# Kernel optimization log

Measured on AMD Instinct MI355X. Metric: run time of the kernel, lower is better.

## Reference

```python
import jax, jax.numpy as jnp
import numpy as np

B, L, E, D, A = 32, 2048, 1024, 1024, 1024

def setup_inputs() -> dict:
    key = jax.random.key(0)
    k1, k2, k3, k4, k5 = jax.random.split(key, 5)
    s_e = 1.0 / np.sqrt(E)
    s_d = 1.0 / np.sqrt(D)
    s_a = 1.0 / np.sqrt(A)
    return {
        "encoder_outputs": jax.random.normal(k1, (B, L, E), dtype=jnp.float32),
        "decoder_hidden": jax.random.normal(k2, (B, D), dtype=jnp.float32),
        "mask": jnp.ones((B, L), dtype=jnp.int32),
        # nn.Linear weights are [out, in]; uniform(-1/sqrt(in), 1/sqrt(in))
        "W1": jax.random.uniform(k3, (A, E), jnp.float32, -s_e, s_e),
        "W2": jax.random.uniform(k4, (A, D), jnp.float32, -s_d, s_d),
        "v": jax.random.uniform(k5, (1, A), jnp.float32, -s_a, s_a),
    }

def reference(encoder_outputs, decoder_hidden, mask, W1, W2, v):
    # enc_t: [B,L,A], dec_t: [B,1,A]
    enc_t = jnp.einsum('ble,ae->bla', encoder_outputs, W1)
    dec_t = jnp.einsum('bd,ad->ba', decoder_hidden, W2)[:, None, :]
    combined = jnp.tanh(enc_t + dec_t)                       # [B,L,A]
    scores = jnp.einsum('bla,a->bl', combined, v[0])          # [B,L]
    scores = jnp.where(mask == 0, -jnp.inf, scores)
    attn = jax.nn.softmax(scores, axis=-1)                    # [B,L]
    context = jnp.einsum('bl,ble->be', attn, encoder_outputs) # [B,E]
    return (context, attn)
```

## Files before the change

kernel.cpp:

```cpp
#include <hip/hip_runtime.h>
#include <stdint.h>

typedef __bf16 bf16x8 __attribute__((ext_vector_type(8)));
typedef float f32x4 __attribute__((ext_vector_type(4)));
typedef unsigned short ushort8v __attribute__((ext_vector_type(8)));

__device__ __forceinline__ void gload_lds16(const void* g, void* l) {
  __builtin_amdgcn_global_load_lds(
      (const __attribute__((address_space(1))) void*)g,
      (__attribute__((address_space(3))) void*)l, 16, 0, 0);
}

__device__ __forceinline__ unsigned short f2bf(float f) {
  union { float f; unsigned int u; } x; x.f = f;
  unsigned int r = x.u + 0x7FFFu + ((x.u >> 16) & 1u);
  return (unsigned short)(r >> 16);
}

__device__ __forceinline__ float ftanh(float x) {
  float ax = fabsf(x);
  float e = __expf(-2.0f * ax);
  float r = (1.0f - e) / (1.0f + e);
  return copysignf(r, x);
}

__global__ __launch_bounds__(256) void w1cvt_kernel(
    const float* __restrict__ W1, unsigned short* __restrict__ w1b) {
  const int g = blockIdx.x * 256 + threadIdx.x;
  const int chunk = g >> 10;
  const int d16 = g & 1023;
  const int col = d16 >> 2, s = d16 & 3;
  const int np = chunk >> 5, ks = chunk & 31;
  const float* src = W1 + (size_t)(np * 256 + col) * 1024 + ks * 32 +
                     ((s ^ ((col >> 1) & 3)) * 8);
  const float4 v0 = *(const float4*)src;
  const float4 v1 = *(const float4*)(src + 4);
  ushort8v o;
  o[0] = f2bf(v0.x); o[1] = f2bf(v0.y); o[2] = f2bf(v0.z); o[3] = f2bf(v0.w);
  o[4] = f2bf(v1.x); o[5] = f2bf(v1.y); o[6] = f2bf(v1.z); o[7] = f2bf(v1.w);
  *((ushort8v*)w1b + g) = o;
}

__global__ __launch_bounds__(256) void dec_proj_kernel(
    const float* __restrict__ dec, const float* __restrict__ W2,
    float* __restrict__ u) {
  __shared__ __align__(16) float w2s[1024];
  const int a = blockIdx.x;
  const int t = threadIdx.x;
  *(float4*)(w2s + t * 4) = *(const float4*)(W2 + (size_t)a * 1024 + t * 4);
  __syncthreads();
  const int wid = t >> 6, l = t & 63;
  for (int bi = 0; bi < 8; ++bi) {
    const int b = wid * 8 + bi;
    const float* dp = dec + (size_t)b * 1024;
    float acc = 0.f;
#pragma unroll
    for (int i = 0; i < 4; ++i) {
      const int k = i * 256 + l * 4;
      const float4 dv = *(const float4*)(dp + k);
      const float4 wv = *(const float4*)(w2s + k);
      acc = fmaf(dv.x, wv.x, acc); acc = fmaf(dv.y, wv.y, acc);
      acc = fmaf(dv.z, wv.z, acc); acc = fmaf(dv.w, wv.w, acc);
    }
#pragma unroll
    for (int m = 1; m < 64; m <<= 1) acc += __shfl_xor(acc, m, 64);
    if (l == 0) u[(size_t)b * 1024 + a] = acc;
  }
}

__global__ __launch_bounds__(256, 2) void scores_kernel(
    const float* __restrict__ enc, const unsigned short* __restrict__ w1b,
    const float* __restrict__ u, const float* __restrict__ vvec,
    float* __restrict__ spart) {
  __shared__ __align__(16) char Al[16384];
  __shared__ __align__(16) char Bl[32768];
  __shared__ __align__(16) float sred[256];

  const int t = threadIdx.x;
  const int bid = blockIdx.x;
  const int np = (bid >> 3) & 3;
  const int panel = (bid & 7) + ((bid >> 5) << 3);
  const int m0 = panel * 128;
  const int n0 = np * 256;
  const int b = panel >> 4;
  const int l = t & 63, wid = t >> 6;
  const int wr = wid >> 1, wc = wid & 1;
  const int lm = l & 15, lg = l >> 4;

  const int soff = (lg ^ ((lm >> 1) & 3)) * 16;
  const int abase = (wr * 64 + lm) * 64 + soff;
  const int bbase = (wc * 128 + lm) * 64 + soff;
  const char* w1base = (const char*)w1b + (size_t)(np * 32) * 16384;
  const float* ub = u + (size_t)b * 1024;

  const int row0 = t >> 2;
  const int s0 = t & 3;
  const int xo = (s0 ^ ((row0 >> 1) & 3)) * 8;
  const float* srcA = enc + (size_t)(m0 + row0) * 1024 + xo;
  const int adst = t * 16;

  f32x4 acc[4][8];
#pragma unroll
  for (int mi = 0; mi < 4; ++mi)
#pragma unroll
    for (int ni = 0; ni < 8; ++ni) acc[mi][ni] = (f32x4){0.f, 0.f, 0.f, 0.f};

#pragma unroll
  for (int i = 0; i < 4; ++i)
    gload_lds16(w1base + i * 4096 + t * 16, Bl + i * 4096 + t * 16);
  {
    const float4 p0 = *(const float4*)srcA;
    const float4 p1 = *(const float4*)(srcA + 4);
    const float4 p2 = *(const float4*)(srcA + 65536);
    const float4 p3 = *(const float4*)(srcA + 65540);
    ushort8v o0, o1;
    o0[0] = f2bf(p0.x); o0[1] = f2bf(p0.y); o0[2] = f2bf(p0.z); o0[3] = f2bf(p0.w);
    o0[4] = f2bf(p1.x); o0[5] = f2bf(p1.y); o0[6] = f2bf(p1.z); o0[7] = f2bf(p1.w);
    o1[0] = f2bf(p2.x); o1[1] = f2bf(p2.y); o1[2] = f2bf(p2.z); o1[3] = f2bf(p2.w);
    o1[4] = f2bf(p3.x); o1[5] = f2bf(p3.y); o1[6] = f2bf(p3.z); o1[7] = f2bf(p3.w);
    *(ushort8v*)(Al + adst) = o0;
    *(ushort8v*)(Al + 4096 + adst) = o1;
  }
  __syncthreads();

#pragma unroll 2
  for (int ks = 0; ks < 32; ++ks) {
    const int abuf = (ks & 1) * 8192;
    const int bbuf = (ks & 1) * 16384;
    float4 p0, p1, p2, p3;
    if (ks < 31) {
      const char* wn = w1base + (size_t)(ks + 1) * 16384;
#pragma unroll
      for (int i = 0; i < 4; ++i)
        gload_lds16(wn + i * 4096 + t * 16,
                    Bl + (bbuf ^ 16384) + i * 4096 + t * 16);
      const float* sa = srcA + (ks + 1) * 32;
      p0 = *(const float4*)sa;
      p1 = *(const float4*)(sa + 4);
      p2 = *(const float4*)(sa + 65536);
      p3 = *(const float4*)(sa + 65540);
    }
    bf16x8 af[4], bf[8];
#pragma unroll
    for (int mi = 0; mi < 4; ++mi)
      af[mi] = *(const bf16x8*)(Al + abuf + abase + mi * 1024);
#pragma unroll
    for (int ni = 0; ni < 8; ++ni)
      bf[ni] = *(const bf16x8*)(Bl + bbuf + bbase + ni * 1024);
    __builtin_amdgcn_s_setprio(1);
#pragma unroll
    for (int mi = 0; mi < 4; ++mi)
#pragma unroll
      for (int ni = 0; ni < 8; ++ni)
        acc[mi][ni] = __builtin_amdgcn_mfma_f32_16x16x32_bf16(
            af[mi], bf[ni], acc[mi][ni], 0, 0, 0);
    __builtin_amdgcn_s_setprio(0);
    if (ks < 31) {
      ushort8v o0, o1;
      o0[0] = f2bf(p0.x); o0[1] = f2bf(p0.y); o0[2] = f2bf(p0.z); o0[3] = f2bf(p0.w);
      o0[4] = f2bf(p1.x); o0[5] = f2bf(p1.y); o0[6] = f2bf(p1.z); o0[7] = f2bf(p1.w);
      o1[0] = f2bf(p2.x); o1[1] = f2bf(p2.y); o1[2] = f2bf(p2.z); o1[3] = f2bf(p2.w);
      o1[4] = f2bf(p3.x); o1[5] = f2bf(p3.y); o1[6] = f2bf(p3.z); o1[7] = f2bf(p3.w);
      *(ushort8v*)(Al + (abuf ^ 8192) + adst) = o0;
      *(ushort8v*)(Al + (abuf ^ 8192) + 4096 + adst) = o1;
    }
    __syncthreads();
  }

  float rowp[4][4];
#pragma unroll
  for (int mi = 0; mi < 4; ++mi)
#pragma unroll
    for (int j = 0; j < 4; ++j) rowp[mi][j] = 0.f;
#pragma unroll
  for (int ni = 0; ni < 8; ++ni) {
    const int colA = n0 + wc * 128 + ni * 16 + lm;
    const float uu = ub[colA], vv = vvec[colA];
#pragma unroll
    for (int mi = 0; mi < 4; ++mi)
#pragma unroll
      for (int j = 0; j < 4; ++j)
        rowp[mi][j] += ftanh(acc[mi][ni][j] + uu) * vv;
  }
#pragma unroll
  for (int m = 1; m < 16; m <<= 1)
#pragma unroll
    for (int mi = 0; mi < 4; ++mi)
#pragma unroll
      for (int j = 0; j < 4; ++j) rowp[mi][j] += __shfl_xor(rowp[mi][j], m, 64);
  if (lm == 0) {
#pragma unroll
    for (int mi = 0; mi < 4; ++mi)
#pragma unroll
      for (int j = 0; j < 4; ++j)
        sred[wc * 128 + wr * 64 + mi * 16 + lg * 4 + j] = rowp[mi][j];
  }
  __syncthreads();
  if (t < 128) {
    spart[(size_t)np * 65536 + m0 + t] = sred[t] + sred[128 + t];
  }
}

__global__ __launch_bounds__(256) void softmax_kernel(
    const float* __restrict__ spart, float* __restrict__ out,
    const int* __restrict__ mask) {
  __shared__ float wred[4];
  const int bidx = blockIdx.x;
  const int t = threadIdx.x;
  const int r8 = bidx * 2048 + t * 8;
  float* at = out + 32768 + (size_t)bidx * 2048;
  const int* mk = mask + (size_t)bidx * 2048;
  float v[8] = {0.f, 0.f, 0.f, 0.f, 0.f, 0.f, 0.f, 0.f};
#pragma unroll
  for (int np = 0; np < 4; ++np) {
    const float4 s0 = *(const float4*)(spart + (size_t)np * 65536 + r8);
    const float4 s1 = *(const float4*)(spart + (size_t)np * 65536 + r8 + 4);
    v[0] += s0.x; v[1] += s0.y; v[2] += s0.z; v[3] += s0.w;
    v[4] += s1.x; v[5] += s1.y; v[6] += s1.z; v[7] += s1.w;
  }
  const int4 q0 = *(const int4*)(mk + t * 8);
  const int4 q1 = *(const int4*)(mk + t * 8 + 4);
  int q[8] = {q0.x, q0.y, q0.z, q0.w, q1.x, q1.y, q1.z, q1.w};
  float mx = -3.0e38f;
#pragma unroll
  for (int j = 0; j < 8; ++j) if (q[j] != 0) mx = fmaxf(mx, v[j]);
#pragma unroll
  for (int m = 1; m < 64; m <<= 1) mx = fmaxf(mx, __shfl_xor(mx, m, 64));
  if ((t & 63) == 0) wred[t >> 6] = mx;
  __syncthreads();
  mx = fmaxf(fmaxf(wred[0], wred[1]), fmaxf(wred[2], wred[3]));
  __syncthreads();
  float pp[8]; float sum = 0.f;
#pragma unroll
  for (int j = 0; j < 8; ++j) {
    pp[j] = (q[j] != 0) ? __expf(v[j] - mx) : 0.f;
    sum += pp[j];
  }
#pragma unroll
  for (int m = 1; m < 64; m <<= 1) sum += __shfl_xor(sum, m, 64);
  if ((t & 63) == 0) wred[t >> 6] = sum;
  __syncthreads();
  sum = (wred[0] + wred[1]) + (wred[2] + wred[3]);
  const float inv = 1.0f / sum;
  const float4 o0 = {pp[0] * inv, pp[1] * inv, pp[2] * inv, pp[3] * inv};
  const float4 o1 = {pp[4] * inv, pp[5] * inv, pp[6] * inv, pp[7] * inv};
  *(float4*)(at + t * 8) = o0;
  *(float4*)(at + t * 8 + 4) = o1;
}

__global__ __launch_bounds__(256) void context_kernel(
    const float* __restrict__ enc, float* __restrict__ out) {
  __shared__ __align__(16) float attnS[2048];
  __shared__ __align__(16) float red[8 * 128];
  const int bid = blockIdx.x;
  const int b = bid >> 3, ec = bid & 7;
  const int e0 = ec * 128;
  const int t = threadIdx.x;
  const float* attn = out + 32768 + (size_t)b * 2048;
#pragma unroll
  for (int i = 0; i < 8; ++i) attnS[i * 256 + t] = attn[i * 256 + t];
  __syncthreads();
  const int el = (t & 31) * 4;
  const int ls = t >> 5;
  f32x4 acc = {0.f, 0.f, 0.f, 0.f};
  const float* ebase = enc + (size_t)b * 2048 * 1024 + e0 + el;
  for (int l2 = ls; l2 < 2048; l2 += 8) {
    const float a = attnS[l2];
    const float4 ev = *(const float4*)(ebase + (size_t)l2 * 1024);
    acc[0] = fmaf(a, ev.x, acc[0]);
    acc[1] = fmaf(a, ev.y, acc[1]);
    acc[2] = fmaf(a, ev.z, acc[2]);
    acc[3] = fmaf(a, ev.w, acc[3]);
  }
  *(f32x4*)(red + ls * 128 + el) = acc;
  __syncthreads();
  if (t < 128) {
    float s = 0.f;
#pragma unroll
    for (int i = 0; i < 8; ++i) s += red[i * 128 + t];
    out[(size_t)b * 1024 + e0 + t] = s;
  }
}

extern "C" void kernel_launch(void* const* d_in, const int* in_sizes, int n_in,
                              void* d_out, int out_size, void* d_ws,
                              size_t ws_size, hipStream_t stream) {
  const float* enc = (const float*)d_in[0];
  const float* dec = (const float*)d_in[1];
  const int* mask = (const int*)d_in[2];
  const float* W1 = (const float*)d_in[3];
  const float* W2 = (const float*)d_in[4];
  const float* v = (const float*)d_in[5];
  float* out = (float*)d_out;
  char* ws = (char*)d_ws;
  unsigned short* w1b = (unsigned short*)ws;
  float* u = (float*)(ws + (2u << 20));
  float* spart = (float*)(ws + (2u << 20) + (128u << 10));

  w1cvt_kernel<<<512, 256, 0, stream>>>(W1, w1b);
  dec_proj_kernel<<<1024, 256, 0, stream>>>(dec, W2, u);
  scores_kernel<<<2048, 256, 0, stream>>>(enc, w1b, u, v, spart);
  softmax_kernel<<<32, 256, 0, stream>>>(spart, out, mask);
  context_kernel<<<256, 256, 0, stream>>>(enc, out);
}
```

Measured before the change: 275.0 us.

## Pre-convert encoder outputs to bf16 and stream them via direct-to-LDS loads

Adds a pass that converts the full fp32 encoder tensor to bf16 in workspace. The scores GEMM then loads A tiles with global_load_lds instead of register loads plus in-loop conversion, and the context reduction reads the bf16 copy. This costs an extra full read of enc (256MB) and a 128MB write, and the context sum now uses bf16-rounded inputs. The new path only runs when the workspace is large enough, otherwise the old kernels run.

```diff
diff --git a/kernel.cpp b/kernel.cpp
--- a/kernel.cpp
+++ b/kernel.cpp
@@ -15,6 +15,11 @@
   union { float f; unsigned int u; } x; x.f = f;
   unsigned int r = x.u + 0x7FFFu + ((x.u >> 16) & 1u);
   return (unsigned short)(r >> 16);
+}
+
+__device__ __forceinline__ float bf2f(unsigned short h) {
+  union { unsigned int u; float f; } x; x.u = ((unsigned int)h) << 16;
+  return x.f;
 }
 
 __device__ __forceinline__ float ftanh(float x) {
@@ -22,6 +27,17 @@
   float e = __expf(-2.0f * ax);
   float r = (1.0f - e) / (1.0f + e);
   return copysignf(r, x);
+}
+
+__global__ __launch_bounds__(256) void enc_cvt_kernel(
+    const float* __restrict__ enc, unsigned short* __restrict__ enc16) {
+  const size_t g = ((size_t)blockIdx.x * 256 + threadIdx.x) * 8;
+  const float4 v0 = *(const float4*)(enc + g);
+  const float4 v1 = *(const float4*)(enc + g + 4);
+  ushort8v o;
+  o[0] = f2bf(v0.x); o[1] = f2bf(v0.y); o[2] = f2bf(v0.z); o[3] = f2bf(v0.w);
+  o[4] = f2bf(v1.x); o[5] = f2bf(v1.y); o[6] = f2bf(v1.z); o[7] = f2bf(v1.w);
+  *(ushort8v*)(enc16 + g) = o;
 }
 
 __global__ __launch_bounds__(256) void w1cvt_kernel(
@@ -68,10 +84,10 @@
   }
 }
 
-__global__ __launch_bounds__(256, 2) void scores_kernel(
-    const float* __restrict__ enc, const unsigned short* __restrict__ w1b,
-    const float* __restrict__ u, const float* __restrict__ vvec,
-    float* __restrict__ spart) {
+__global__ __launch_bounds__(256, 2) void scores_kernel_g(
+    const unsigned short* __restrict__ enc16,
+    const unsigned short* __restrict__ w1b, const float* __restrict__ u,
+    const float* __restrict__ vvec, float* __restrict__ spart) {
   __shared__ __align__(16) char Al[16384];
   __shared__ __align__(16) char Bl[32768];
   __shared__ __align__(16) float sred[256];
@@ -93,18 +109,122 @@
   const char* w1base = (const char*)w1b + (size_t)(np * 32) * 16384;
   const float* ub = u + (size_t)b * 1024;
 
+  const int row1 = t >> 2, slot1 = t & 3;
+  const char* asrc1 = (const char*)enc16 + (size_t)(m0 + row1) * 2048 +
+                      ((slot1 ^ ((row1 >> 1) & 3)) * 16);
+  const char* asrc2 = asrc1 + 64 * 2048;
+
+  f32x4 acc[4][8];
+#pragma unroll
+  for (int mi = 0; mi < 4; ++mi)
+#pragma unroll
+    for (int ni = 0; ni < 8; ++ni) acc[mi][ni] = (f32x4){0.f, 0.f, 0.f, 0.f};
+
+#pragma unroll
+  for (int i = 0; i < 4; ++i)
+    gload_lds16(w1base + i * 4096 + t * 16, Bl + i * 4096 + t * 16);
+  gload_lds16(asrc1, Al + t * 16);
+  gload_lds16(asrc2, Al + 4096 + t * 16);
+  __syncthreads();
+
+#pragma unroll 2
+  for (int ks = 0; ks < 32; ++ks) {
+    const int abuf = (ks & 1) * 8192;
+    const int bbuf = (ks & 1) * 16384;
+    if (ks < 31) {
+      const char* wn = w1base + (size_t)(ks + 1) * 16384;
+#pragma unroll
+      for (int i = 0; i < 4; ++i)
+        gload_lds16(wn + i * 4096 + t * 16,
+                    Bl + (bbuf ^ 16384) + i * 4096 + t * 16);
+      const int aoff = (ks + 1) * 64;
+      gload_lds16(asrc1 + aoff, Al + (abuf ^ 8192) + t * 16);
+      gload_lds16(asrc2 + aoff, Al + (abuf ^ 8192) + 4096 + t * 16);
+    }
+    bf16x8 af[4], bf[8];
+#pragma unroll
+    for (int mi = 0; mi < 4; ++mi)
+      af[mi] = *(const bf16x8*)(Al + abuf + abase + mi * 1024);
+#pragma unroll
+    for (int ni = 0; ni < 8; ++ni)
+      bf[ni] = *(const bf16x8*)(Bl + bbuf + bbase + ni * 1024);
+    __builtin_amdgcn_s_setprio(1);
+#pragma unroll
+    for (int mi = 0; mi < 4; ++mi)
+#pragma unroll
+      for (int ni = 0; ni < 8; ++ni)
+        acc[mi][ni] = __builtin_amdgcn_mfma_f32_16x16x32_bf16(
+            af[mi], bf[ni], acc[mi][ni], 0, 0, 0);
+    __builtin_amdgcn_s_setprio(0);
+    __syncthreads();
+  }
+
+  float rowp[4][4];
+#pragma unroll
+  for (int mi = 0; mi < 4; ++mi)
+#pragma unroll
+    for (int j = 0; j < 4; ++j) rowp[mi][j] = 0.f;
+#pragma unroll
+  for (int ni = 0; ni < 8; ++ni) {
+    const int colA = n0 + wc * 128 + ni * 16 + lm;
+    const float uu = ub[colA], vv = vvec[colA];
+#pragma unroll
+    for (int mi = 0; mi < 4; ++mi)
+#pragma unroll
+      for (int j = 0; j < 4; ++j)
+        rowp[mi][j] += ftanh(acc[mi][ni][j] + uu) * vv;
+  }
+#pragma unroll
+  for (int m = 1; m < 16; m <<= 1)
+#pragma unroll
+    for (int mi = 0; mi < 4; ++mi)
+#pragma unroll
+      for (int j = 0; j < 4; ++j) rowp[mi][j] += __shfl_xor(rowp[mi][j], m, 64);
+  if (lm == 0) {
+#pragma unroll
+    for (int mi = 0; mi < 4; ++mi)
+#pragma unroll
+      for (int j = 0; j < 4; ++j)
+        sred[wc * 128 + wr * 64 + mi * 16 + lg * 4 + j] = rowp[mi][j];
+  }
+  __syncthreads();
+  if (t < 128) {
+    spart[(size_t)np * 65536 + m0 + t] = sred[t] + sred[128 + t];
+  }
+}
+
+__global__ __launch_bounds__(256, 2) void scores_kernel(
+    const float* __restrict__ enc, const unsigned short* __restrict__ w1b,
+    const float* __restrict__ u, const float* __restrict__ vvec,
+    float* __restrict__ spart) {
+  __shared__ __align__(16) char Al[16384];
+  __shared__ __align__(16) char Bl[32768];
+  __shared__ __align__(16) float sred[256];
+  const int t = threadIdx.x;
+  const int bid = blockIdx.x;
+  const int np = (bid >> 3) & 3;
+  const int panel = (bid & 7) + ((bid >> 5) << 3);
+  const int m0 = panel * 128;
+  const int n0 = np * 256;
+  const int b = panel >> 4;
+  const int l = t & 63, wid = t >> 6;
+  const int wr = wid >> 1, wc = wid & 1;
+  const int lm = l & 15, lg = l >> 4;
+  const int soff = (lg ^ ((lm >> 1) & 3)) * 16;
+  const int abase = (wr * 64 + lm) * 64 + soff;
+  const int bbase = (wc * 128 + lm) * 64 + soff;
+  const char* w1base = (const char*)w1b + (size_t)(np * 32) * 16384;
+  const float* ub = u + (size_t)b * 1024;
   const int row0 = t >> 2;
   const int s0 = t & 3;
   const int xo = (s0 ^ ((row0 >> 1) & 3)) * 8;
   const float* srcA = enc + (size_t)(m0 + row0) * 1024 + xo;
   const int adst = t * 16;
-
   f32x4 acc[4][8];
 #pragma unroll
   for (int mi = 0; mi < 4; ++mi)
 #pragma unroll
     for (int ni = 0; ni < 8; ++ni) acc[mi][ni] = (f32x4){0.f, 0.f, 0.f, 0.f};
-
 #pragma unroll
   for (int i = 0; i < 4; ++i)
     gload_lds16(w1base + i * 4096 + t * 16, Bl + i * 4096 + t * 16);
@@ -122,7 +242,6 @@
     *(ushort8v*)(Al + 4096 + adst) = o1;
   }
   __syncthreads();
-
 #pragma unroll 2
   for (int ks = 0; ks < 32; ++ks) {
     const int abuf = (ks & 1) * 8192;
@@ -166,7 +285,6 @@
     }
     __syncthreads();
   }
-
   float rowp[4][4];
 #pragma unroll
   for (int mi = 0; mi < 4; ++mi)
@@ -246,6 +364,41 @@
   const float4 o1 = {pp[4] * inv, pp[5] * inv, pp[6] * inv, pp[7] * inv};
   *(float4*)(at + t * 8) = o0;
   *(float4*)(at + t * 8 + 4) = o1;
+}
+
+__global__ __launch_bounds__(256) void context16_kernel(
+    const unsigned short* __restrict__ enc16, float* __restrict__ out) {
+  __shared__ __align__(16) float attnS[2048];
+  __shared__ __align__(16) float red[16 * 132];
+  const int bid = blockIdx.x;
+  const int b = bid >> 3, ec = bid & 7;
+  const int e0 = ec * 128;
+  const int t = threadIdx.x;
+  const float* attn = out + 32768 + (size_t)b * 2048;
+#pragma unroll
+  for (int i = 0; i < 8; ++i) attnS[i * 256 + t] = attn[i * 256 + t];
+  __syncthreads();
+  const int el = (t & 15) * 8;
+  const int ls = t >> 4;
+  float acc[8];
+#pragma unroll
+  for (int j = 0; j < 8; ++j) acc[j] = 0.f;
+  const unsigned short* eb = enc16 + (size_t)b * 2048 * 1024 + e0 + el;
+  for (int l2 = ls; l2 < 2048; l2 += 16) {
+    const float a = attnS[l2];
+    const ushort8v ev = *(const ushort8v*)(eb + (size_t)l2 * 1024);
+#pragma unroll
+    for (int j = 0; j < 8; ++j) acc[j] = fmaf(a, bf2f(ev[j]), acc[j]);
+  }
+#pragma unroll
+  for (int j = 0; j < 8; ++j) red[ls * 132 + el + j] = acc[j];
+  __syncthreads();
+  if (t < 128) {
+    float s = 0.f;
+#pragma unroll
+    for (int i = 0; i < 16; ++i) s += red[i * 132 + t];
+    out[(size_t)b * 1024 + e0 + t] = s;
+  }
 }
 
 __global__ __launch_bounds__(256) void context_kernel(
@@ -294,12 +447,22 @@
   float* out = (float*)d_out;
   char* ws = (char*)d_ws;
   unsigned short* w1b = (unsigned short*)ws;
-  float* u = (float*)(ws + (2u << 20));
-  float* spart = (float*)(ws + (2u << 20) + (128u << 10));
+  float* u = (float*)(ws + 2097152);
+  float* spart = (float*)(ws + 2097152 + 131072);
+  unsigned short* enc16 =
+      (unsigned short*)(ws + 2097152 + 131072 + 1048576);
+  const size_t NEED = 2097152ull + 131072ull + 1048576ull + 134217728ull;
 
   w1cvt_kernel<<<512, 256, 0, stream>>>(W1, w1b);
   dec_proj_kernel<<<1024, 256, 0, stream>>>(dec, W2, u);
-  scores_kernel<<<2048, 256, 0, stream>>>(enc, w1b, u, v, spart);
-  softmax_kernel<<<32, 256, 0, stream>>>(spart, out, mask);
-  context_kernel<<<256, 256, 0, stream>>>(enc, out);
-}
+  if (ws_size >= NEED) {
+    enc_cvt_kernel<<<32768, 256, 0, stream>>>(enc, enc16);
+    scores_kernel_g<<<2048, 256, 0, stream>>>(enc16, w1b, u, v, spart);
+    softmax_kernel<<<32, 256, 0, stream>>>(spart, out, mask);
+    context16_kernel<<<256, 256, 0, stream>>>(enc16, out);
+  } else {
+    scores_kernel<<<2048, 256, 0, stream>>>(enc, w1b, u, v, spart);
+    softmax_kernel<<<32, 256, 0, stream>>>(spart, out, mask);
+    context_kernel<<<256, 256, 0, stream>>>(enc, out);
+  }
+}
```

After: 283.1 us. +2.9%, slower.

## Pre-convert encoder outputs to bf16 and use larger 256x256 score tiles

Applied to the files above, without the earlier changes.

Adds a separate pass that converts encoder_outputs to a bf16 copy in workspace. The scores GEMM can then stream A tiles straight into LDS with global_load_lds instead of converting fp32 in registers. The scores kernel grows to 512 threads with a 256x256 tile, and its sync becomes an explicit vmcnt wait plus barrier. The context kernel now reads the bf16 copy, halving its bytes. In exchange there is an extra full read and write pass over the encoder tensor, a large workspace requirement, and lower precision in the context reduction.

```diff
diff --git a/kernel.cpp b/kernel.cpp
--- a/kernel.cpp
+++ b/kernel.cpp
@@ -15,6 +15,11 @@
   union { float f; unsigned int u; } x; x.f = f;
   unsigned int r = x.u + 0x7FFFu + ((x.u >> 16) & 1u);
   return (unsigned short)(r >> 16);
+}
+
+__device__ __forceinline__ float bf2f(unsigned short h) {
+  union { unsigned int u; float f; } x; x.u = ((unsigned int)h) << 16;
+  return x.f;
 }
 
 __device__ __forceinline__ float ftanh(float x) {
@@ -22,6 +27,21 @@
   float e = __expf(-2.0f * ax);
   float r = (1.0f - e) / (1.0f + e);
   return copysignf(r, x);
+}
+
+__device__ __forceinline__ int swz4(int r) {
+  return (r & 3) ^ ((r >> 2) & 3);
+}
+
+__global__ __launch_bounds__(256) void enc_cvt_kernel(
+    const float* __restrict__ enc, unsigned short* __restrict__ enc16) {
+  const size_t g = ((size_t)blockIdx.x * 256 + threadIdx.x) * 8;
+  const float4 v0 = *(const float4*)(enc + g);
+  const float4 v1 = *(const float4*)(enc + g + 4);
+  ushort8v o;
+  o[0] = f2bf(v0.x); o[1] = f2bf(v0.y); o[2] = f2bf(v0.z); o[3] = f2bf(v0.w);
+  o[4] = f2bf(v1.x); o[5] = f2bf(v1.y); o[6] = f2bf(v1.z); o[7] = f2bf(v1.w);
+  *(ushort8v*)(enc16 + g) = o;
 }
 
 __global__ __launch_bounds__(256) void w1cvt_kernel(
@@ -30,9 +50,9 @@
   const int chunk = g >> 10;
   const int d16 = g & 1023;
   const int col = d16 >> 2, s = d16 & 3;
-  const int np = chunk >> 5, ks = chunk & 31;
-  const float* src = W1 + (size_t)(np * 256 + col) * 1024 + ks * 32 +
-                     ((s ^ ((col >> 1) & 3)) * 8);
+  const int np = chunk >> 5, kt = chunk & 31;
+  const float* src = W1 + (size_t)(np * 256 + col) * 1024 + kt * 32 +
+                     ((s ^ swz4(col)) * 8);
   const float4 v0 = *(const float4*)src;
   const float4 v1 = *(const float4*)(src + 4);
   ushort8v o;
@@ -68,116 +88,90 @@
   }
 }
 
-__global__ __launch_bounds__(256, 2) void scores_kernel(
-    const float* __restrict__ enc, const unsigned short* __restrict__ w1b,
-    const float* __restrict__ u, const float* __restrict__ vvec,
-    float* __restrict__ spart) {
-  __shared__ __align__(16) char Al[16384];
+__global__ __launch_bounds__(512, 2) void scores8_kernel(
+    const unsigned short* __restrict__ enc16,
+    const unsigned short* __restrict__ w1b, const float* __restrict__ u,
+    const float* __restrict__ vvec, float* __restrict__ spart) {
+  __shared__ __align__(16) char Al[32768];
   __shared__ __align__(16) char Bl[32768];
-  __shared__ __align__(16) float sred[256];
 
   const int t = threadIdx.x;
   const int bid = blockIdx.x;
   const int np = (bid >> 3) & 3;
   const int panel = (bid & 7) + ((bid >> 5) << 3);
-  const int m0 = panel * 128;
-  const int n0 = np * 256;
-  const int b = panel >> 4;
+  const int m0 = panel * 256;
+  const int b = panel >> 3;
   const int l = t & 63, wid = t >> 6;
-  const int wr = wid >> 1, wc = wid & 1;
+  const int wr = wid >> 2, wc = wid & 3;
   const int lm = l & 15, lg = l >> 4;
 
-  const int soff = (lg ^ ((lm >> 1) & 3)) * 16;
-  const int abase = (wr * 64 + lm) * 64 + soff;
-  const int bbase = (wc * 128 + lm) * 64 + soff;
+  const int koff = (lg << 4) ^ (swz4(lm) << 4);
+  const int abase = (wr * 128 + lm) * 64 + koff;
+  const int bbase = (wc * 64 + lm) * 64 + koff;
   const char* w1base = (const char*)w1b + (size_t)(np * 32) * 16384;
   const float* ub = u + (size_t)b * 1024;
 
-  const int row0 = t >> 2;
-  const int s0 = t & 3;
-  const int xo = (s0 ^ ((row0 >> 1) & 3)) * 8;
-  const float* srcA = enc + (size_t)(m0 + row0) * 1024 + xo;
-  const int adst = t * 16;
-
-  f32x4 acc[4][8];
-#pragma unroll
-  for (int mi = 0; mi < 4; ++mi)
-#pragma unroll
-    for (int ni = 0; ni < 8; ++ni) acc[mi][ni] = (f32x4){0.f, 0.f, 0.f, 0.f};
-
-#pragma unroll
-  for (int i = 0; i < 4; ++i)
-    gload_lds16(w1base + i * 4096 + t * 16, Bl + i * 4096 + t * 16);
-  {
-    const float4 p0 = *(const float4*)srcA;
-    const float4 p1 = *(const float4*)(srcA + 4);
-    const float4 p2 = *(const float4*)(srcA + 65536);
-    const float4 p3 = *(const float4*)(srcA + 65540);
-    ushort8v o0, o1;
-    o0[0] = f2bf(p0.x); o0[1] = f2bf(p0.y); o0[2] = f2bf(p0.z); o0[3] = f2bf(p0.w);
-    o0[4] = f2bf(p1.x); o0[5] = f2bf(p1.y); o0[6] = f2bf(p1.z); o0[7] = f2bf(p1.w);
-    o1[0] = f2bf(p2.x); o1[1] = f2bf(p2.y); o1[2] = f2bf(p2.z); o1[3] = f2bf(p2.w);
-    o1[4] = f2bf(p3.x); o1[5] = f2bf(p3.y); o1[6] = f2bf(p3.z); o1[7] = f2bf(p3.w);
-    *(ushort8v*)(Al + adst) = o0;
-    *(ushort8v*)(Al + 4096 + adst) = o1;
-  }
+  const int idx0 = t, idx1 = t + 512;
+  const int ar0 = idx0 >> 2, as0 = idx0 & 3;
+  const int ar1 = idx1 >> 2, as1 = idx1 & 3;
+  const char* aS0 = (const char*)enc16 + (size_t)(m0 + ar0) * 2048 +
+                    ((as0 ^ swz4(ar0)) * 16);
+  const char* aS1 = (const char*)enc16 + (size_t)(m0 + ar1) * 2048 +
+                    ((as1 ^ swz4(ar1)) * 16);
+
+  f32x4 acc[8][4];
+#pragma unroll
+  for (int mi = 0; mi < 8; ++mi)
+#pragma unroll
+    for (int ni = 0; ni < 4; ++ni) acc[mi][ni] = (f32x4){0.f, 0.f, 0.f, 0.f};
+
+  gload_lds16(w1base + idx0 * 16, Bl + idx0 * 16);
+  gload_lds16(w1base + idx1 * 16, Bl + idx1 * 16);
+  gload_lds16(aS0, Al + idx0 * 16);
+  gload_lds16(aS1, Al + idx1 * 16);
   __syncthreads();
 
 #pragma unroll 2
-  for (int ks = 0; ks < 32; ++ks) {
-    const int abuf = (ks & 1) * 8192;
-    const int bbuf = (ks & 1) * 16384;
-    float4 p0, p1, p2, p3;
-    if (ks < 31) {
-      const char* wn = w1base + (size_t)(ks + 1) * 16384;
-#pragma unroll
-      for (int i = 0; i < 4; ++i)
-        gload_lds16(wn + i * 4096 + t * 16,
-                    Bl + (bbuf ^ 16384) + i * 4096 + t * 16);
-      const float* sa = srcA + (ks + 1) * 32;
-      p0 = *(const float4*)sa;
-      p1 = *(const float4*)(sa + 4);
-      p2 = *(const float4*)(sa + 65536);
-      p3 = *(const float4*)(sa + 65540);
+  for (int kt = 0; kt < 32; ++kt) {
+    const int buf = (kt & 1) * 16384;
+    const int nbuf = buf ^ 16384;
+    if (kt < 31) {
+      const char* wn = w1base + (size_t)(kt + 1) * 16384;
+      const int ao = (kt + 1) * 64;
+      gload_lds16(wn + idx0 * 16, Bl + nbuf + idx0 * 16);
+      gload_lds16(wn + idx1 * 16, Bl + nbuf + idx1 * 16);
+      gload_lds16(aS0 + ao, Al + nbuf + idx0 * 16);
+      gload_lds16(aS1 + ao, Al + nbuf + idx1 * 16);
     }
-    bf16x8 af[4], bf[8];
-#pragma unroll
-    for (int mi = 0; mi < 4; ++mi)
-      af[mi] = *(const bf16x8*)(Al + abuf + abase + mi * 1024);
-#pragma unroll
-    for (int ni = 0; ni < 8; ++ni)
-      bf[ni] = *(const bf16x8*)(Bl + bbuf + bbase + ni * 1024);
+    bf16x8 bfr[4];
+#pragma unroll
+    for (int ni = 0; ni < 4; ++ni)
+      bfr[ni] = *(const bf16x8*)(Bl + buf + bbase + ni * 1024);
     __builtin_amdgcn_s_setprio(1);
 #pragma unroll
-    for (int mi = 0; mi < 4; ++mi)
-#pragma unroll
-      for (int ni = 0; ni < 8; ++ni)
+    for (int mi = 0; mi < 8; ++mi) {
+      const bf16x8 afr = *(const bf16x8*)(Al + buf + abase + mi * 1024);
+#pragma unroll
+      for (int ni = 0; ni < 4; ++ni)
         acc[mi][ni] = __builtin_amdgcn_mfma_f32_16x16x32_bf16(
-            af[mi], bf[ni], acc[mi][ni], 0, 0, 0);
+            afr, bfr[ni], acc[mi][ni], 0, 0, 0);
+    }
     __builtin_amdgcn_s_setprio(0);
-    if (ks < 31) {
-      ushort8v o0, o1;
-      o0[0] = f2bf(p0.x); o0[1] = f2bf(p0.y); o0[2] = f2bf(p0.z); o0[3] = f2bf(p0.w);
-      o0[4] = f2bf(p1.x); o0[5] = f2bf(p1.y); o0[6] = f2bf(p1.z); o0[7] = f2bf(p1.w);
-      o1[0] = f2bf(p2.x); o1[1] = f2bf(p2.y); o1[2] = f2bf(p2.z); o1[3] = f2bf(p2.w);
-      o1[4] = f2bf(p3.x); o1[5] = f2bf(p3.y); o1[6] = f2bf(p3.z); o1[7] = f2bf(p3.w);
-      *(ushort8v*)(Al + (abuf ^ 8192) + adst) = o0;
-      *(ushort8v*)(Al + (abuf ^ 8192) + 4096 + adst) = o1;
-    }
-    __syncthreads();
-  }
-
-  float rowp[4][4];
-#pragma unroll
-  for (int mi = 0; mi < 4; ++mi)
+    asm volatile("s_waitcnt vmcnt(0)" ::: "memory");
+    __builtin_amdgcn_s_barrier();
+  }
+
+  float rowp[8][4];
+#pragma unroll
+  for (int mi = 0; mi < 8; ++mi)
 #pragma unroll
     for (int j = 0; j < 4; ++j) rowp[mi][j] = 0.f;
 #pragma unroll
-  for (int ni = 0; ni < 8; ++ni) {
-    const int colA = n0 + wc * 128 + ni * 16 + lm;
+  for (int ni = 0; ni < 4; ++ni) {
+    const int colA = np * 256 + wc * 64 + ni * 16 + lm;
     const float uu = ub[colA], vv = vvec[colA];
 #pragma unroll
-    for (int mi = 0; mi < 4; ++mi)
+    for (int mi = 0; mi < 8; ++mi)
 #pragma unroll
       for (int j = 0; j < 4; ++j)
         rowp[mi][j] += ftanh(acc[mi][ni][j] + uu) * vv;
@@ -185,19 +179,21 @@
 #pragma unroll
   for (int m = 1; m < 16; m <<= 1)
 #pragma unroll
-    for (int mi = 0; mi < 4; ++mi)
+    for (int mi = 0; mi < 8; ++mi)
 #pragma unroll
       for (int j = 0; j < 4; ++j) rowp[mi][j] += __shfl_xor(rowp[mi][j], m, 64);
+  float* sred = (float*)Al;
   if (lm == 0) {
 #pragma unroll
-    for (int mi = 0; mi < 4; ++mi)
+    for (int mi = 0; mi < 8; ++mi)
 #pragma unroll
       for (int j = 0; j < 4; ++j)
-        sred[wc * 128 + wr * 64 + mi * 16 + lg * 4 + j] = rowp[mi][j];
-  }
-  __syncthreads();
-  if (t < 128) {
-    spart[(size_t)np * 65536 + m0 + t] = sred[t] + sred[128 + t];
+        sred[wc * 256 + wr * 128 + mi * 16 + lg * 4 + j] = rowp[mi][j];
+  }
+  __syncthreads();
+  if (t < 256) {
+    spart[(size_t)np * 65536 + m0 + t] =
+        sred[t] + sred[256 + t] + sred[512 + t] + sred[768 + t];
   }
 }
 
@@ -248,10 +244,10 @@
   *(float4*)(at + t * 8 + 4) = o1;
 }
 
-__global__ __launch_bounds__(256) void context_kernel(
-    const float* __restrict__ enc, float* __restrict__ out) {
+__global__ __launch_bounds__(256) void context16_kernel(
+    const unsigned short* __restrict__ enc16, float* __restrict__ out) {
   __shared__ __align__(16) float attnS[2048];
-  __shared__ __align__(16) float red[8 * 128];
+  __shared__ __align__(16) float red[16 * 132];
   const int bid = blockIdx.x;
   const int b = bid >> 3, ec = bid & 7;
   const int e0 = ec * 128;
@@ -260,24 +256,25 @@
 #pragma unroll
   for (int i = 0; i < 8; ++i) attnS[i * 256 + t] = attn[i * 256 + t];
   __syncthreads();
-  const int el = (t & 31) * 4;
-  const int ls = t >> 5;
-  f32x4 acc = {0.f, 0.f, 0.f, 0.f};
-  const float* ebase = enc + (size_t)b * 2048 * 1024 + e0 + el;
-  for (int l2 = ls; l2 < 2048; l2 += 8) {
+  const int el = (t & 15) * 8;
+  const int ls = t >> 4;
+  float acc[8];
+#pragma unroll
+  for (int j = 0; j < 8; ++j) acc[j] = 0.f;
+  const unsigned short* eb = enc16 + (size_t)b * 2048 * 1024 + e0 + el;
+  for (int l2 = ls; l2 < 2048; l2 += 16) {
     const float a = attnS[l2];
-    const float4 ev = *(const float4*)(ebase + (size_t)l2 * 1024);
-    acc[0] = fmaf(a, ev.x, acc[0]);
-    acc[1] = fmaf(a, ev.y, acc[1]);
-    acc[2] = fmaf(a, ev.z, acc[2]);
-    acc[3] = fmaf(a, ev.w, acc[3]);
-  }
-  *(f32x4*)(red + ls * 128 + el) = acc;
+    const ushort8v ev = *(const ushort8v*)(eb + (size_t)l2 * 1024);
+#pragma unroll
+    for (int j = 0; j < 8; ++j) acc[j] = fmaf(a, bf2f(ev[j]), acc[j]);
+  }
+#pragma unroll
+  for (int j = 0; j < 8; ++j) red[ls * 132 + el + j] = acc[j];
   __syncthreads();
   if (t < 128) {
     float s = 0.f;
 #pragma unroll
-    for (int i = 0; i < 8; ++i) s += red[i * 128 + t];
+    for (int i = 0; i < 16; ++i) s += red[i * 132 + t];
     out[(size_t)b * 1024 + e0 + t] = s;
   }
 }
@@ -294,12 +291,15 @@
   float* out = (float*)d_out;
   char* ws = (char*)d_ws;
   unsigned short* w1b = (unsigned short*)ws;
-  float* u = (float*)(ws + (2u << 20));
-  float* spart = (float*)(ws + (2u << 20) + (128u << 10));
+  float* u = (float*)(ws + 2097152);
+  float* spart = (float*)(ws + 2097152 + 131072);
+  unsigned short* enc16 =
+      (unsigned short*)(ws + 2097152 + 131072 + 1048576);
 
   w1cvt_kernel<<<512, 256, 0, stream>>>(W1, w1b);
   dec_proj_kernel<<<1024, 256, 0, stream>>>(dec, W2, u);
-  scores_kernel<<<2048, 256, 0, stream>>>(enc, w1b, u, v, spart);
+  enc_cvt_kernel<<<32768, 256, 0, stream>>>(enc, enc16);
+  scores8_kernel<<<1024, 512, 0, stream>>>(enc16, w1b, u, v, spart);
   softmax_kernel<<<32, 256, 0, stream>>>(spart, out, mask);
-  context_kernel<<<256, 256, 0, stream>>>(enc, out);
-}
+  context16_kernel<<<256, 256, 0, stream>>>(enc16, out);
+}
```

Result: slower. 336.8 us (+22.5%).

## Widen scores GEMM tile to 512 columns with 8-wave blocks

Applied to the files above, without the earlier changes.

The scores kernel now covers 512 attention columns per block instead of 256, using 512 threads (8 waves arranged 2x4) and half as many blocks. Each encoder tile is therefore loaded and converted to bf16 two times instead of four, which cuts redundant global reads of the large encoder tensor and the number of partial-score planes the softmax has to sum. The weight pre-conversion layout is changed to match the wider panels. In exchange, LDS use per block grows (64KB B buffer, with the A buffer reused for the reduction), which may lower occupancy, and the grid has fewer blocks.

```diff
diff --git a/kernel.cpp b/kernel.cpp
--- a/kernel.cpp
+++ b/kernel.cpp
@@ -27,11 +27,11 @@
 __global__ __launch_bounds__(256) void w1cvt_kernel(
     const float* __restrict__ W1, unsigned short* __restrict__ w1b) {
   const int g = blockIdx.x * 256 + threadIdx.x;
-  const int chunk = g >> 10;
-  const int d16 = g & 1023;
-  const int col = d16 >> 2, s = d16 & 3;
-  const int np = chunk >> 5, ks = chunk & 31;
-  const float* src = W1 + (size_t)(np * 256 + col) * 1024 + ks * 32 +
+  const int chunk = g >> 11;
+  const int d = g & 2047;
+  const int col = d >> 2, s = d & 3;
+  const int np = chunk >> 5, kt = chunk & 31;
+  const float* src = W1 + (size_t)(np * 512 + col) * 1024 + kt * 32 +
                      ((s ^ ((col >> 1) & 3)) * 8);
   const float4 v0 = *(const float4*)src;
   const float4 v1 = *(const float4*)(src + 4);
@@ -68,29 +68,27 @@
   }
 }
 
-__global__ __launch_bounds__(256, 2) void scores_kernel(
+__global__ __launch_bounds__(512, 2) void scores_kernel(
     const float* __restrict__ enc, const unsigned short* __restrict__ w1b,
     const float* __restrict__ u, const float* __restrict__ vvec,
     float* __restrict__ spart) {
   __shared__ __align__(16) char Al[16384];
-  __shared__ __align__(16) char Bl[32768];
-  __shared__ __align__(16) float sred[256];
+  __shared__ __align__(16) char Bl[65536];
 
   const int t = threadIdx.x;
   const int bid = blockIdx.x;
-  const int np = (bid >> 3) & 3;
-  const int panel = (bid & 7) + ((bid >> 5) << 3);
+  const int np = (bid >> 3) & 1;
+  const int panel = (bid & 7) | ((bid >> 4) << 3);
   const int m0 = panel * 128;
-  const int n0 = np * 256;
   const int b = panel >> 4;
   const int l = t & 63, wid = t >> 6;
-  const int wr = wid >> 1, wc = wid & 1;
+  const int wr = wid >> 2, wc = wid & 3;
   const int lm = l & 15, lg = l >> 4;
 
   const int soff = (lg ^ ((lm >> 1) & 3)) * 16;
   const int abase = (wr * 64 + lm) * 64 + soff;
   const int bbase = (wc * 128 + lm) * 64 + soff;
-  const char* w1base = (const char*)w1b + (size_t)(np * 32) * 16384;
+  const char* w1base = (const char*)w1b + (size_t)np * 1048576;
   const float* ub = u + (size_t)b * 1024;
 
   const int row0 = t >> 2;
@@ -107,38 +105,31 @@
 
 #pragma unroll
   for (int i = 0; i < 4; ++i)
-    gload_lds16(w1base + i * 4096 + t * 16, Bl + i * 4096 + t * 16);
+    gload_lds16(w1base + (i * 512 + t) * 16, Bl + (i * 512 + t) * 16);
   {
     const float4 p0 = *(const float4*)srcA;
     const float4 p1 = *(const float4*)(srcA + 4);
-    const float4 p2 = *(const float4*)(srcA + 65536);
-    const float4 p3 = *(const float4*)(srcA + 65540);
-    ushort8v o0, o1;
-    o0[0] = f2bf(p0.x); o0[1] = f2bf(p0.y); o0[2] = f2bf(p0.z); o0[3] = f2bf(p0.w);
-    o0[4] = f2bf(p1.x); o0[5] = f2bf(p1.y); o0[6] = f2bf(p1.z); o0[7] = f2bf(p1.w);
-    o1[0] = f2bf(p2.x); o1[1] = f2bf(p2.y); o1[2] = f2bf(p2.z); o1[3] = f2bf(p2.w);
-    o1[4] = f2bf(p3.x); o1[5] = f2bf(p3.y); o1[6] = f2bf(p3.z); o1[7] = f2bf(p3.w);
-    *(ushort8v*)(Al + adst) = o0;
-    *(ushort8v*)(Al + 4096 + adst) = o1;
+    ushort8v o;
+    o[0] = f2bf(p0.x); o[1] = f2bf(p0.y); o[2] = f2bf(p0.z); o[3] = f2bf(p0.w);
+    o[4] = f2bf(p1.x); o[5] = f2bf(p1.y); o[6] = f2bf(p1.z); o[7] = f2bf(p1.w);
+    *(ushort8v*)(Al + adst) = o;
   }
   __syncthreads();
 
 #pragma unroll 2
-  for (int ks = 0; ks < 32; ++ks) {
-    const int abuf = (ks & 1) * 8192;
-    const int bbuf = (ks & 1) * 16384;
-    float4 p0, p1, p2, p3;
-    if (ks < 31) {
-      const char* wn = w1base + (size_t)(ks + 1) * 16384;
+  for (int kt = 0; kt < 32; ++kt) {
+    const int abuf = (kt & 1) * 8192;
+    const int bbuf = (kt & 1) * 32768;
+    float4 p0, p1;
+    if (kt < 31) {
+      const char* wn = w1base + (size_t)(kt + 1) * 32768;
 #pragma unroll
       for (int i = 0; i < 4; ++i)
-        gload_lds16(wn + i * 4096 + t * 16,
-                    Bl + (bbuf ^ 16384) + i * 4096 + t * 16);
-      const float* sa = srcA + (ks + 1) * 32;
+        gload_lds16(wn + (i * 512 + t) * 16,
+                    Bl + (bbuf ^ 32768) + (i * 512 + t) * 16);
+      const float* sa = srcA + (kt + 1) * 32;
       p0 = *(const float4*)sa;
       p1 = *(const float4*)(sa + 4);
-      p2 = *(const float4*)(sa + 65536);
-      p3 = *(const float4*)(sa + 65540);
     }
     bf16x8 af[4], bf[8];
 #pragma unroll
@@ -155,14 +146,11 @@
         acc[mi][ni] = __builtin_amdgcn_mfma_f32_16x16x32_bf16(
             af[mi], bf[ni], acc[mi][ni], 0, 0, 0);
     __builtin_amdgcn_s_setprio(0);
-    if (ks < 31) {
-      ushort8v o0, o1;
-      o0[0] = f2bf(p0.x); o0[1] = f2bf(p0.y); o0[2] = f2bf(p0.z); o0[3] = f2bf(p0.w);
-      o0[4] = f2bf(p1.x); o0[5] = f2bf(p1.y); o0[6] = f2bf(p1.z); o0[7] = f2bf(p1.w);
-      o1[0] = f2bf(p2.x); o1[1] = f2bf(p2.y); o1[2] = f2bf(p2.z); o1[3] = f2bf(p2.w);
-      o1[4] = f2bf(p3.x); o1[5] = f2bf(p3.y); o1[6] = f2bf(p3.z); o1[7] = f2bf(p3.w);
-      *(ushort8v*)(Al + (abuf ^ 8192) + adst) = o0;
-      *(ushort8v*)(Al + (abuf ^ 8192) + 4096 + adst) = o1;
+    if (kt < 31) {
+      ushort8v o;
+      o[0] = f2bf(p0.x); o[1] = f2bf(p0.y); o[2] = f2bf(p0.z); o[3] = f2bf(p0.w);
+      o[4] = f2bf(p1.x); o[5] = f2bf(p1.y); o[6] = f2bf(p1.z); o[7] = f2bf(p1.w);
+      *(ushort8v*)(Al + (abuf ^ 8192) + adst) = o;
     }
     __syncthreads();
   }
@@ -174,7 +162,7 @@
     for (int j = 0; j < 4; ++j) rowp[mi][j] = 0.f;
 #pragma unroll
   for (int ni = 0; ni < 8; ++ni) {
-    const int colA = n0 + wc * 128 + ni * 16 + lm;
+    const int colA = np * 512 + wc * 128 + ni * 16 + lm;
     const float uu = ub[colA], vv = vvec[colA];
 #pragma unroll
     for (int mi = 0; mi < 4; ++mi)
@@ -188,6 +176,7 @@
     for (int mi = 0; mi < 4; ++mi)
 #pragma unroll
       for (int j = 0; j < 4; ++j) rowp[mi][j] += __shfl_xor(rowp[mi][j], m, 64);
+  float* sred = (float*)Al;
   if (lm == 0) {
 #pragma unroll
     for (int mi = 0; mi < 4; ++mi)
@@ -197,7 +186,8 @@
   }
   __syncthreads();
   if (t < 128) {
-    spart[(size_t)np * 65536 + m0 + t] = sred[t] + sred[128 + t];
+    spart[(size_t)np * 65536 + m0 + t] =
+        sred[t] + sred[128 + t] + sred[256 + t] + sred[384 + t];
   }
 }
 
@@ -210,13 +200,15 @@
   const int r8 = bidx * 2048 + t * 8;
   float* at = out + 32768 + (size_t)bidx * 2048;
   const int* mk = mask + (size_t)bidx * 2048;
-  float v[8] = {0.f, 0.f, 0.f, 0.f, 0.f, 0.f, 0.f, 0.f};
-#pragma unroll
-  for (int np = 0; np < 4; ++np) {
-    const float4 s0 = *(const float4*)(spart + (size_t)np * 65536 + r8);
-    const float4 s1 = *(const float4*)(spart + (size_t)np * 65536 + r8 + 4);
-    v[0] += s0.x; v[1] += s0.y; v[2] += s0.z; v[3] += s0.w;
-    v[4] += s1.x; v[5] += s1.y; v[6] += s1.z; v[7] += s1.w;
+  float v[8];
+  {
+    const float4 s0 = *(const float4*)(spart + r8);
+    const float4 s1 = *(const float4*)(spart + r8 + 4);
+    const float4 s2 = *(const float4*)(spart + 65536 + r8);
+    const float4 s3 = *(const float4*)(spart + 65536 + r8 + 4);
+    v[0] = s0.x + s2.x; v[1] = s0.y + s2.y; v[2] = s0.z + s2.z;
+    v[3] = s0.w + s2.w; v[4] = s1.x + s3.x; v[5] = s1.y + s3.y;
+    v[6] = s1.z + s3.z; v[7] = s1.w + s3.w;
   }
   const int4 q0 = *(const int4*)(mk + t * 8);
   const int4 q1 = *(const int4*)(mk + t * 8 + 4);
@@ -294,12 +286,12 @@
   float* out = (float*)d_out;
   char* ws = (char*)d_ws;
   unsigned short* w1b = (unsigned short*)ws;
-  float* u = (float*)(ws + (2u << 20));
-  float* spart = (float*)(ws + (2u << 20) + (128u << 10));
+  float* u = (float*)(ws + 2097152);
+  float* spart = (float*)(ws + 2097152 + 131072);
 
   w1cvt_kernel<<<512, 256, 0, stream>>>(W1, w1b);
   dec_proj_kernel<<<1024, 256, 0, stream>>>(dec, W2, u);
-  scores_kernel<<<2048, 256, 0, stream>>>(enc, w1b, u, v, spart);
+  scores_kernel<<<1024, 512, 0, stream>>>(enc, w1b, u, v, spart);
   softmax_kernel<<<32, 256, 0, stream>>>(spart, out, mask);
   context_kernel<<<256, 256, 0, stream>>>(enc, out);
 }
```

New measurement: 271.6 us, median of 2. About the same (-1.2%).
